# Kernel tuning notes

Measured on AMD Instinct MI355X. Metric: run time of the kernel, lower is better.

Reference implementation:

```python
import jax, jax.numpy as jnp
import numpy as np

HEADS = 16

def setup_inputs() -> dict:
    key = jax.random.key(0)
    ks = jax.random.split(key, 12)
    S, E = 2048, 1024
    x = jax.random.normal(ks[0], (S, E), dtype=jnp.float32)
    seg = jnp.sort(jax.random.randint(ks[1], (S,), 0, 32)).astype(jnp.int32)
    sc = 1.0 / np.sqrt(E)
    Wq = jax.random.normal(ks[2], (E, E), dtype=jnp.float32) * sc
    bq = jax.random.normal(ks[3], (E,), dtype=jnp.float32) * 0.01
    Wk = jax.random.normal(ks[4], (E, E), dtype=jnp.float32) * sc
    bk = jax.random.normal(ks[5], (E,), dtype=jnp.float32) * 0.01
    Wv = jax.random.normal(ks[6], (E, E), dtype=jnp.float32) * sc
    bv = jax.random.normal(ks[7], (E,), dtype=jnp.float32) * 0.01
    Wo = jax.random.normal(ks[8], (E, E), dtype=jnp.float32) * sc
    bo = jax.random.normal(ks[9], (E,), dtype=jnp.float32) * 0.01
    return {"x": x, "seg": seg, "pos": 1000,
            "Wq": Wq, "bq": bq, "Wk": Wk, "bk": bk,
            "Wv": Wv, "bv": bv, "Wo": Wo, "bo": bo}

def reference(x, seg, pos, Wq, bq, Wk, bk, Wv, bv, Wo, bo):
    S, E = x.shape
    H = HEADS
    d = E // H
    # projections: [S,E] -> [H,S,d]
    q = (x @ Wq + bq).reshape(S, H, d).transpose(1, 0, 2)
    k = (x @ Wk + bk).reshape(S, H, d).transpose(1, 0, 2)
    v = (x @ Wv + bv).reshape(S, H, d).transpose(1, 0, 2)
    # raw scores (note: original code applies NO 1/sqrt(d) scaling)
    scores = jnp.einsum('hid,hjd->hij', q, k)  # [H,S,S]
    same_seg = seg[:, None] == seg[None, :]    # [S,S]
    # faithful to original: out-of-segment entries stay ZERO (not -inf)
    scores = jnp.where(same_seg[None, :, :], scores, 0.0)
    weights = jax.nn.softmax(scores, axis=-1)
    out = jnp.einsum('hij,hjd->hid', weights, v)          # [H,S,d]
    out = out.transpose(1, 0, 2).reshape(S, E)            # [S,E]
    result = out @ Wo + bo                                # [S,E]
    # mean over the segment containing `pos`
    m = (seg == seg[pos]).astype(result.dtype)            # [S]
    return (result * m[:, None]).sum(axis=0) / m.sum()
```

## Files before the change

### kernel.cpp

```cpp
#include <hip/hip_runtime.h>

#define SS 2048
#define EE 1024
#define NH 16
#define DH 64
#define NR 128


__device__ __forceinline__ void fma4v(float4& a, const float4 xv,
                                      const float4 w0, const float4 w1,
                                      const float4 w2, const float4 w3) {
    a.x += xv.x * w0.x + xv.y * w1.x + xv.z * w2.x + xv.w * w3.x;
    a.y += xv.x * w0.y + xv.y * w1.y + xv.z * w2.y + xv.w * w3.y;
    a.z += xv.x * w0.z + xv.y * w1.z + xv.z * w2.z + xv.w * w3.z;
    a.w += xv.x * w0.w + xv.y * w1.w + xv.z * w2.w + xv.w * w3.w;
}

__device__ __forceinline__ void lgkm_wait() {
    asm volatile("s_waitcnt lgkmcnt(0)" ::: "memory");
}

__device__ __forceinline__ int2 seg_bounds(const int* __restrict__ seg,
                                           const int* __restrict__ pos) {
    __shared__ int sb[8];
    int t = threadIdx.x;
    int g = seg[pos[0]];
    int lomin = SS, himax = 0;
    const int4* s4 = (const int4*)seg;
#pragma unroll
    for (int i = t; i < SS / 4; i += 256) {
        int4 v = s4[i];
        int b = i * 4;
        if (v.x == g) { lomin = min(lomin, b);     himax = max(himax, b + 1); }
        if (v.y == g) { lomin = min(lomin, b + 1); himax = max(himax, b + 2); }
        if (v.z == g) { lomin = min(lomin, b + 2); himax = max(himax, b + 3); }
        if (v.w == g) { lomin = min(lomin, b + 3); himax = max(himax, b + 4); }
    }
    for (int o = 32; o; o >>= 1) {
        lomin = min(lomin, __shfl_xor(lomin, o, 64));
        himax = max(himax, __shfl_xor(himax, o, 64));
    }
    if ((t & 63) == 0) { sb[t >> 6] = lomin; sb[4 + (t >> 6)] = himax; }
    __syncthreads();
    return make_int2(min(min(sb[0], sb[1]), min(sb[2], sb[3])),
                     max(max(sb[4], sb[5]), max(sb[6], sb[7])));
}

__global__ void __launch_bounds__(256, 4) k_d1(
    const float* __restrict__ x, const int* __restrict__ seg,
    const int* __restrict__ pos,
    const float* __restrict__ Wq, const float* __restrict__ bq,
    const float* __restrict__ Wk, const float* __restrict__ bk,
    const float* __restrict__ Wv, const float* __restrict__ bv,
    float* __restrict__ xpart,
    float* __restrict__ Q, float* __restrict__ K, float* __restrict__ V,
    int nmax) {
    __shared__ float lds[4096];
    const int t = threadIdx.x, wv = t >> 6, lane = t & 63;

    if (blockIdx.z == 0) {
        int xb = blockIdx.y * 16 + blockIdx.x;
        if (xb >= 64) return;
        const float4* x4 = (const float4*)x + (size_t)(xb * 32) * 256 + t;
        float4 a = make_float4(0.f, 0.f, 0.f, 0.f);
#pragma unroll 8
        for (int r = 0; r < 32; ++r) {
            float4 v = x4[(size_t)r * 256];
            a.x += v.x; a.y += v.y; a.z += v.z; a.w += v.w;
        }
        ((float4*)(xpart + (size_t)xb * EE))[t] = a;
        return;
    }

    int2 bnd = seg_bounds(seg, pos);
    int lo = bnd.x;
    int nc = bnd.y - lo; if (nc > nmax) nc = nmax; if (nc < 1) nc = 1;
    int r0 = blockIdx.y * 4;
    if (r0 >= nc) return;
    int mat = blockIdx.z - 1;
    const float* W  = mat == 0 ? Wq : mat == 1 ? Wk : Wv;
    const float* bb = mat == 0 ? bq : mat == 1 ? bk : bv;
    float* dst      = mat == 0 ? Q  : mat == 1 ? K  : V;
    int e = blockIdx.x * 64 + lane;

    float (*xs)[1024] = (float(*)[1024])lds;
    int rw = r0 + wv; if (rw >= nc) rw = nc - 1;
    {
        const float4* src = (const float4*)(x + (size_t)(lo + rw) * EE);
        float4* dl = (float4*)&xs[wv][0];
#pragma unroll
        for (int i = 0; i < 4; ++i)
            dl[i * 64 + lane] = src[i * 64 + lane];
    }
    __syncthreads();

    const float* Wp = W + (size_t)(wv * 256) * EE + e;
    const float* x0 = &xs[0][wv * 256];
    const float* x1 = &xs[1][wv * 256];
    const float* x2 = &xs[2][wv * 256];
    const float* x3 = &xs[3][wv * 256];
    float a0 = 0.f, a1 = 0.f, a2 = 0.f, a3 = 0.f;
#pragma unroll 8
    for (int c = 0; c < 256; ++c) {
        float wj = Wp[(size_t)c * EE];
        a0 += x0[c] * wj;
        a1 += x1[c] * wj;
        a2 += x2[c] * wj;
        a3 += x3[c] * wj;
    }
    __syncthreads();

    float* red = lds;
    red[(wv * 4 + 0) * 64 + lane] = a0;
    red[(wv * 4 + 1) * 64 + lane] = a1;
    red[(wv * 4 + 2) * 64 + lane] = a2;
    red[(wv * 4 + 3) * 64 + lane] = a3;
    __syncthreads();
    float s = red[(0 * 4 + wv) * 64 + lane] + red[(1 * 4 + wv) * 64 + lane]
            + red[(2 * 4 + wv) * 64 + lane] + red[(3 * 4 + wv) * 64 + lane]
            + bb[e];
    int gr = r0 + wv;
    if (gr < nc)
        dst[(size_t)gr * EE + e] = s;
}

__global__ void __launch_bounds__(256, 4) k_d2(
    const int* __restrict__ seg, const int* __restrict__ pos,
    const float* __restrict__ Wv, const float* __restrict__ bv,
    const float* __restrict__ xpart,
    const float* __restrict__ Q, const float* __restrict__ K,
    const float* __restrict__ V,
    float* __restrict__ vtot, float* __restrict__ A, float* __restrict__ Bh,
    int nmax) {
    __shared__ float lds[2048];
    const int t = threadIdx.x, wv = t >> 6, lane = t & 63;
    const int bid = blockIdx.x, gb = gridDim.x;

    if (bid < 4) {
        float4 a = make_float4(0.f, 0.f, 0.f, 0.f);
        const float4* xp4 = (const float4*)xpart + t;
#pragma unroll 8
        for (int b = 0; b < 64; ++b) {
            float4 v = xp4[(size_t)b * 256];
            a.x += v.x; a.y += v.y; a.z += v.z; a.w += v.w;
        }
        ((float4*)lds)[t] = a;
        __syncthreads();
        int ct = bid;
        int e0 = ct * 256 + lane * 4;
        const float* Wp = Wv + (size_t)(wv * 256) * EE + e0;
        const float* xs = lds + wv * 256;
        float4 acc = make_float4(0.f, 0.f, 0.f, 0.f);
#pragma unroll 2
        for (int c = 0; c < 256; c += 4) {
            float4 w0 = *(const float4*)(Wp + (size_t)(c + 0) * EE);
            float4 w1 = *(const float4*)(Wp + (size_t)(c + 1) * EE);
            float4 w2 = *(const float4*)(Wp + (size_t)(c + 2) * EE);
            float4 w3 = *(const float4*)(Wp + (size_t)(c + 3) * EE);
            float4 xv = *(const float4*)(xs + c);
            fma4v(acc, xv, w0, w1, w2, w3);
        }
        *(float4*)(lds + 1024 + wv * 256 + lane * 4) = acc;
        __syncthreads();
        if (t < 64) {
            int oc = t * 4;
            float4 s0 = *(float4*)(lds + 1024 + 0 * 256 + oc);
            float4 s1 = *(float4*)(lds + 1024 + 1 * 256 + oc);
            float4 s2 = *(float4*)(lds + 1024 + 2 * 256 + oc);
            float4 s3 = *(float4*)(lds + 1024 + 3 * 256 + oc);
            float4 bvv = *(const float4*)(bv + ct * 256 + oc);
            float4 s;
            s.x = s0.x + s1.x + s2.x + s3.x + bvv.x * (float)SS;
            s.y = s0.y + s1.y + s2.y + s3.y + bvv.y * (float)SS;
            s.z = s0.z + s1.z + s2.z + s3.z + bvv.z * (float)SS;
            s.w = s0.w + s1.w + s2.w + s3.w + bvv.w * (float)SS;
            *(float4*)(vtot + ct * 256 + oc) = s;
        }
        return;
    }

    int2 bnd = seg_bounds(seg, pos);
    int nc = bnd.y - bnd.x; if (nc > nmax) nc = nmax; if (nc < 1) nc = 1;
    int nit = nc * NH;
    float* ql = lds + wv * 512;
    float* sb = ql + 64;
    for (int it = (bid - 4) * 4 + wv; it < nit; it += (gb - 4) * 4) {
        int r = it >> 4, h = it & 15;
        ql[lane] = Q[(size_t)r * EE + h * DH + lane];
        lgkm_wait();
        const float4* q4 = (const float4*)ql;
        float m = 0.f;
        for (int j = lane; j < nc; j += 64) {
            const float4* kr = (const float4*)(K + (size_t)j * EE + h * DH);
            float s = 0.f;
#pragma unroll 4
            for (int d = 0; d < DH / 4; ++d) {
                float4 kv = kr[d];
                float4 qv = q4[d];
                s += qv.x * kv.x + qv.y * kv.y + qv.z * kv.z + qv.w * kv.w;
            }
            sb[j] = s;
            m = fmaxf(m, s);
        }
        for (int o = 32; o; o >>= 1) m = fmaxf(m, __shfl_xor(m, o, 64));
        float dl = 0.f;
        for (int j = lane; j < nc; j += 64) {
            float wgt = __expf(sb[j] - m);
            sb[j] = wgt;
            dl += wgt;
        }
        for (int o = 32; o; o >>= 1) dl += __shfl_xor(dl, o, 64);
        float em = __expf(-m);
        float denom = dl + (float)(SS - nc) * em;
        lgkm_wait();
        float acc = 0.f, vs = 0.f;
        const float* Vp = V + h * DH + lane;
        int j = 0;
        for (; j + 4 <= nc; j += 4) {
            float4 wq = *(const float4*)(sb + j);
            float v0 = Vp[(size_t)(j + 0) * EE];
            float v1 = Vp[(size_t)(j + 1) * EE];
            float v2 = Vp[(size_t)(j + 2) * EE];
            float v3 = Vp[(size_t)(j + 3) * EE];
            acc += wq.x * v0 + wq.y * v1 + wq.z * v2 + wq.w * v3;
            vs  += v0 + v1 + v2 + v3;
        }
        for (; j < nc; ++j) {
            float v0 = Vp[(size_t)j * EE];
            acc += sb[j] * v0;
            vs  += v0;
        }
        atomicAdd(&A[h * DH + lane], (acc - vs * em) / denom);
        if (lane == 0) atomicAdd(&Bh[h], em / denom);
    }
}

__global__ void __launch_bounds__(256, 2) k_d3(
    const int* __restrict__ seg, const int* __restrict__ pos,
    const float* __restrict__ Wo, const float* __restrict__ bo,
    const float* __restrict__ vtot, const float* __restrict__ A,
    const float* __restrict__ Bh, int nmax, float* __restrict__ out) {
    __shared__ float lds[2048];
    const int t = threadIdx.x, wv = t >> 6, lane = t & 63;
    int2 bnd = seg_bounds(seg, pos);
    int nc = bnd.y - bnd.x; if (nc > nmax) nc = nmax; if (nc < 1) nc = 1;
    {
        float4 av = ((const float4*)A)[t];
        float4 vv = ((const float4*)vtot)[t];
        float bh = Bh[t >> 4];
        float4 o4;
        o4.x = av.x + vv.x * bh;
        o4.y = av.y + vv.y * bh;
        o4.z = av.z + vv.z * bh;
        o4.w = av.w + vv.w * bh;
        ((float4*)lds)[t] = o4;
    }
    __syncthreads();
    int ct = blockIdx.x;
    int e0 = ct * 256 + lane * 4;
    const float* Wp = Wo + (size_t)(wv * 256) * EE + e0;
    const float* osp = lds + wv * 256;
    float4 a = make_float4(0.f, 0.f, 0.f, 0.f);
#pragma unroll 2
    for (int c = 0; c < 256; c += 4) {
        float4 w0 = *(const float4*)(Wp + (size_t)(c + 0) * EE);
        float4 w1 = *(const float4*)(Wp + (size_t)(c + 1) * EE);
        float4 w2 = *(const float4*)(Wp + (size_t)(c + 2) * EE);
        float4 w3 = *(const float4*)(Wp + (size_t)(c + 3) * EE);
        float4 ov = *(const float4*)(osp + c);
        fma4v(a, ov, w0, w1, w2, w3);
    }
    *(float4*)(lds + 1024 + wv * 256 + lane * 4) = a;
    __syncthreads();
    if (t < 64) {
        int oc = t * 4;
        float4 s0 = *(float4*)(lds + 1024 + 0 * 256 + oc);
        float4 s1 = *(float4*)(lds + 1024 + 1 * 256 + oc);
        float4 s2 = *(float4*)(lds + 1024 + 2 * 256 + oc);
        float4 s3 = *(float4*)(lds + 1024 + 3 * 256 + oc);
        float inv = 1.f / (float)nc;
        float4 bov = *(const float4*)(bo + ct * 256 + oc);
        float4 o;
        o.x = bov.x + (s0.x + s1.x + s2.x + s3.x) * inv;
        o.y = bov.y + (s0.y + s1.y + s2.y + s3.y) * inv;
        o.z = bov.z + (s0.z + s1.z + s2.z + s3.z) * inv;
        o.w = bov.w + (s0.w + s1.w + s2.w + s3.w) * inv;
        *(float4*)(out + ct * 256 + oc) = o;
    }
}

extern "C" void kernel_launch(void* const* d_in, const int* in_sizes, int n_in,
                              void* d_out, int out_size, void* d_ws, size_t ws_size,
                              hipStream_t stream) {
    const float* x  = (const float*)d_in[0];
    const int* seg  = (const int*)d_in[1];
    const int* pos  = (const int*)d_in[2];
    const float* Wq = (const float*)d_in[3];
    const float* bq = (const float*)d_in[4];
    const float* Wk = (const float*)d_in[5];
    const float* bk = (const float*)d_in[6];
    const float* Wv = (const float*)d_in[7];
    const float* bv = (const float*)d_in[8];
    const float* Wo = (const float*)d_in[9];
    const float* bo = (const float*)d_in[10];
    float* out = (float*)d_out;

    char* w = (char*)d_ws;
    float* vtot  = (float*)(w + 0);
    float* A     = (float*)(w + 4096);
    float* Bh    = (float*)(w + 8192);
    float* xpart = (float*)(w + 16384);

    size_t base = 16384 + 64 * EE * sizeof(float);
    size_t avail = (ws_size > base) ? ws_size - base : 0;
    int nmax = (int)(avail / (3ull * EE * sizeof(float)));
    if (nmax > NR) nmax = NR;
    if (nmax < 1) nmax = 1;
    float* Q = (float*)(w + base);
    float* K = Q + (size_t)nmax * EE;
    float* V = K + (size_t)nmax * EE;

    int RT = (nmax + 3) / 4;
    int RY = RT > 4 ? RT : 4;

    hipMemsetAsync(w + 4096, 0, 8192, stream);
    k_d1<<<dim3(16, RY, 4), 256, 0, stream>>>(
        x, seg, pos, Wq, bq, Wk, bk, Wv, bv, xpart, Q, K, V, nmax);
    k_d2<<<260, 256, 0, stream>>>(
        seg, pos, Wv, bv, xpart, Q, K, V, vtot, A, Bh, nmax);
    k_d3<<<4, 256, 0, stream>>>(seg, pos, Wo, bo, vtot, A, Bh, nmax, out);
}
```

Measured before the change: 157.3 us.

## Replace x partial-sum buffer with atomics, precompute segment bounds, widen d2/d3 grids

The column sum of x is now accumulated with global atomics into one vector instead of 64 partial rows that k_d2 had to reduce. A dedicated block in k_d1 computes the segment bounds once and stores them in workspace, so k_d2 and k_d3 no longer rescan seg. The QKV projection reads x rows straight from global memory with wave-uniform addresses rather than staging them in LDS, and it loops over row tiles on a fixed 16-row-tile grid. The Wv and Wo matvecs are split over 16 blocks of 64 columns each, up from 4 blocks, to spread the weight streaming across more CUs. This adds atomic contention and makes the floating-point summation order nondeterministic.

Result: no change. 157.6 us (+0.2%).

```diff
diff --git a/kernel.cpp b/kernel.cpp
--- a/kernel.cpp
+++ b/kernel.cpp
@@ -7,17 +7,8 @@
 #define NR 128
 
 
-__device__ __forceinline__ void fma4v(float4& a, const float4 xv,
-                                      const float4 w0, const float4 w1,
-                                      const float4 w2, const float4 w3) {
-    a.x += xv.x * w0.x + xv.y * w1.x + xv.z * w2.x + xv.w * w3.x;
-    a.y += xv.x * w0.y + xv.y * w1.y + xv.z * w2.y + xv.w * w3.y;
-    a.z += xv.x * w0.z + xv.y * w1.z + xv.z * w2.z + xv.w * w3.z;
-    a.w += xv.x * w0.w + xv.y * w1.w + xv.z * w2.w + xv.w * w3.w;
-}
-
-__device__ __forceinline__ void lgkm_wait() {
-    asm volatile("s_waitcnt lgkmcnt(0)" ::: "memory");
+__device__ __forceinline__ int rfl(int v) {
+    return __builtin_amdgcn_readfirstlane(v);
 }
 
 __device__ __forceinline__ int2 seg_bounds(const int* __restrict__ seg,
@@ -52,82 +43,82 @@
     const float* __restrict__ Wq, const float* __restrict__ bq,
     const float* __restrict__ Wk, const float* __restrict__ bk,
     const float* __restrict__ Wv, const float* __restrict__ bv,
-    float* __restrict__ xpart,
+    float* __restrict__ xsum, int* __restrict__ meta,
     float* __restrict__ Q, float* __restrict__ K, float* __restrict__ V,
     int nmax) {
-    __shared__ float lds[4096];
+    __shared__ float red[1024];
     const int t = threadIdx.x, wv = t >> 6, lane = t & 63;
 
     if (blockIdx.z == 0) {
         int xb = blockIdx.y * 16 + blockIdx.x;
-        if (xb >= 64) return;
-        const float4* x4 = (const float4*)x + (size_t)(xb * 32) * 256 + t;
-        float4 a = make_float4(0.f, 0.f, 0.f, 0.f);
+        if (xb < 64) {
+            const float4* x4 = (const float4*)x + (size_t)(xb * 32) * 256 + t;
+            float4 a = make_float4(0.f, 0.f, 0.f, 0.f);
 #pragma unroll 8
-        for (int r = 0; r < 32; ++r) {
-            float4 v = x4[(size_t)r * 256];
-            a.x += v.x; a.y += v.y; a.z += v.z; a.w += v.w;
-        }
-        ((float4*)(xpart + (size_t)xb * EE))[t] = a;
+            for (int r = 0; r < 32; ++r) {
+                float4 v = x4[(size_t)r * 256];
+                a.x += v.x; a.y += v.y; a.z += v.z; a.w += v.w;
+            }
+            int e0 = 4 * t;
+            atomicAdd(&xsum[e0 + 0], a.x);
+            atomicAdd(&xsum[e0 + 1], a.y);
+            atomicAdd(&xsum[e0 + 2], a.z);
+            atomicAdd(&xsum[e0 + 3], a.w);
+        } else if (xb == 64) {
+            int2 bnd = seg_bounds(seg, pos);
+            if (t == 0) { meta[0] = bnd.x; meta[1] = bnd.y; }
+        }
         return;
     }
 
     int2 bnd = seg_bounds(seg, pos);
     int lo = bnd.x;
     int nc = bnd.y - lo; if (nc > nmax) nc = nmax; if (nc < 1) nc = 1;
-    int r0 = blockIdx.y * 4;
-    if (r0 >= nc) return;
     int mat = blockIdx.z - 1;
     const float* W  = mat == 0 ? Wq : mat == 1 ? Wk : Wv;
     const float* bb = mat == 0 ? bq : mat == 1 ? bk : bv;
     float* dst      = mat == 0 ? Q  : mat == 1 ? K  : V;
     int e = blockIdx.x * 64 + lane;
-
-    float (*xs)[1024] = (float(*)[1024])lds;
-    int rw = r0 + wv; if (rw >= nc) rw = nc - 1;
-    {
-        const float4* src = (const float4*)(x + (size_t)(lo + rw) * EE);
-        float4* dl = (float4*)&xs[wv][0];
-#pragma unroll
-        for (int i = 0; i < 4; ++i)
-            dl[i * 64 + lane] = src[i * 64 + lane];
-    }
-    __syncthreads();
-
-    const float* Wp = W + (size_t)(wv * 256) * EE + e;
-    const float* x0 = &xs[0][wv * 256];
-    const float* x1 = &xs[1][wv * 256];
-    const float* x2 = &xs[2][wv * 256];
-    const float* x3 = &xs[3][wv * 256];
-    float a0 = 0.f, a1 = 0.f, a2 = 0.f, a3 = 0.f;
+    int kbu = rfl(wv) * 256;
+    const float* Wp = W + (size_t)kbu * EE + e;
+    float bias = bb[e];
+
+    for (int rt = blockIdx.y; rt * 4 < nc; rt += 16) {
+        int r0 = rt * 4;
+        int rB = min(r0 + 1, nc - 1);
+        int rC = min(r0 + 2, nc - 1);
+        int rD = min(r0 + 3, nc - 1);
+        const float* xA = x + (size_t)rfl(lo + r0) * EE + kbu;
+        const float* xB = x + (size_t)rfl(lo + rB) * EE + kbu;
+        const float* xC = x + (size_t)rfl(lo + rC) * EE + kbu;
+        const float* xD = x + (size_t)rfl(lo + rD) * EE + kbu;
+        float a0 = 0.f, a1 = 0.f, a2 = 0.f, a3 = 0.f;
 #pragma unroll 8
-    for (int c = 0; c < 256; ++c) {
-        float wj = Wp[(size_t)c * EE];
-        a0 += x0[c] * wj;
-        a1 += x1[c] * wj;
-        a2 += x2[c] * wj;
-        a3 += x3[c] * wj;
-    }
-    __syncthreads();
-
-    float* red = lds;
-    red[(wv * 4 + 0) * 64 + lane] = a0;
-    red[(wv * 4 + 1) * 64 + lane] = a1;
-    red[(wv * 4 + 2) * 64 + lane] = a2;
-    red[(wv * 4 + 3) * 64 + lane] = a3;
-    __syncthreads();
-    float s = red[(0 * 4 + wv) * 64 + lane] + red[(1 * 4 + wv) * 64 + lane]
-            + red[(2 * 4 + wv) * 64 + lane] + red[(3 * 4 + wv) * 64 + lane]
-            + bb[e];
-    int gr = r0 + wv;
-    if (gr < nc)
-        dst[(size_t)gr * EE + e] = s;
+        for (int c = 0; c < 256; ++c) {
+            float wj = Wp[(size_t)c * EE];
+            a0 += xA[c] * wj;
+            a1 += xB[c] * wj;
+            a2 += xC[c] * wj;
+            a3 += xD[c] * wj;
+        }
+        __syncthreads();
+        red[(wv * 4 + 0) * 64 + lane] = a0;
+        red[(wv * 4 + 1) * 64 + lane] = a1;
+        red[(wv * 4 + 2) * 64 + lane] = a2;
+        red[(wv * 4 + 3) * 64 + lane] = a3;
+        __syncthreads();
+        float s = red[(0 * 4 + wv) * 64 + lane] + red[(1 * 4 + wv) * 64 + lane]
+                + red[(2 * 4 + wv) * 64 + lane] + red[(3 * 4 + wv) * 64 + lane]
+                + bias;
+        int gr = r0 + wv;
+        if (gr < nc)
+            dst[(size_t)gr * EE + e] = s;
+    }
 }
 
 __global__ void __launch_bounds__(256, 4) k_d2(
-    const int* __restrict__ seg, const int* __restrict__ pos,
     const float* __restrict__ Wv, const float* __restrict__ bv,
-    const float* __restrict__ xpart,
+    const float* __restrict__ xsum, const int* __restrict__ meta,
     const float* __restrict__ Q, const float* __restrict__ K,
     const float* __restrict__ V,
     float* __restrict__ vtot, float* __restrict__ A, float* __restrict__ Bh,
@@ -136,58 +127,42 @@
     const int t = threadIdx.x, wv = t >> 6, lane = t & 63;
     const int bid = blockIdx.x, gb = gridDim.x;
 
-    if (bid < 4) {
-        float4 a = make_float4(0.f, 0.f, 0.f, 0.f);
-        const float4* xp4 = (const float4*)xpart + t;
-#pragma unroll 8
-        for (int b = 0; b < 64; ++b) {
-            float4 v = xp4[(size_t)b * 256];
-            a.x += v.x; a.y += v.y; a.z += v.z; a.w += v.w;
-        }
-        ((float4*)lds)[t] = a;
-        __syncthreads();
-        int ct = bid;
-        int e0 = ct * 256 + lane * 4;
-        const float* Wp = Wv + (size_t)(wv * 256) * EE + e0;
-        const float* xs = lds + wv * 256;
-        float4 acc = make_float4(0.f, 0.f, 0.f, 0.f);
-#pragma unroll 2
+    if (bid < 16) {
+        ((float4*)lds)[t] = ((const float4*)xsum)[t];
+        __syncthreads();
+        int e = bid * 64 + lane;
+        int kbu = rfl(wv) * 256;
+        const float* Wp = Wv + (size_t)kbu * EE + e;
+        const float4* xs4 = (const float4*)(lds + kbu);
+        float a = 0.f;
+#pragma unroll 4
         for (int c = 0; c < 256; c += 4) {
-            float4 w0 = *(const float4*)(Wp + (size_t)(c + 0) * EE);
-            float4 w1 = *(const float4*)(Wp + (size_t)(c + 1) * EE);
-            float4 w2 = *(const float4*)(Wp + (size_t)(c + 2) * EE);
-            float4 w3 = *(const float4*)(Wp + (size_t)(c + 3) * EE);
-            float4 xv = *(const float4*)(xs + c);
-            fma4v(acc, xv, w0, w1, w2, w3);
-        }
-        *(float4*)(lds + 1024 + wv * 256 + lane * 4) = acc;
-        __syncthreads();
-        if (t < 64) {
-            int oc = t * 4;
-            float4 s0 = *(float4*)(lds + 1024 + 0 * 256 + oc);
-            float4 s1 = *(float4*)(lds + 1024 + 1 * 256 + oc);
-            float4 s2 = *(float4*)(lds + 1024 + 2 * 256 + oc);
-            float4 s3 = *(float4*)(lds + 1024 + 3 * 256 + oc);
-            float4 bvv = *(const float4*)(bv + ct * 256 + oc);
-            float4 s;
-            s.x = s0.x + s1.x + s2.x + s3.x + bvv.x * (float)SS;
-            s.y = s0.y + s1.y + s2.y + s3.y + bvv.y * (float)SS;
-            s.z = s0.z + s1.z + s2.z + s3.z + bvv.z * (float)SS;
-            s.w = s0.w + s1.w + s2.w + s3.w + bvv.w * (float)SS;
-            *(float4*)(vtot + ct * 256 + oc) = s;
+            float4 xv = xs4[c >> 2];
+            a += xv.x * Wp[(size_t)(c + 0) * EE]
+               + xv.y * Wp[(size_t)(c + 1) * EE]
+               + xv.z * Wp[(size_t)(c + 2) * EE]
+               + xv.w * Wp[(size_t)(c + 3) * EE];
+        }
+        __syncthreads();
+        lds[1024 + wv * 64 + lane] = a;
+        __syncthreads();
+        if (wv == 0) {
+            float s = lds[1024 + lane] + lds[1088 + lane]
+                    + lds[1152 + lane] + lds[1216 + lane];
+            vtot[e] = s + bv[e] * (float)SS;
         }
         return;
     }
 
-    int2 bnd = seg_bounds(seg, pos);
-    int nc = bnd.y - bnd.x; if (nc > nmax) nc = nmax; if (nc < 1) nc = 1;
+    int lo = meta[0];
+    int nc = meta[1] - lo; if (nc > nmax) nc = nmax; if (nc < 1) nc = 1;
     int nit = nc * NH;
     float* ql = lds + wv * 512;
     float* sb = ql + 64;
-    for (int it = (bid - 4) * 4 + wv; it < nit; it += (gb - 4) * 4) {
+    for (int it = (bid - 16) * 4 + wv; it < nit; it += (gb - 16) * 4) {
         int r = it >> 4, h = it & 15;
         ql[lane] = Q[(size_t)r * EE + h * DH + lane];
-        lgkm_wait();
+        asm volatile("s_waitcnt lgkmcnt(0)" ::: "memory");
         const float4* q4 = (const float4*)ql;
         float m = 0.f;
         for (int j = lane; j < nc; j += 64) {
@@ -212,7 +187,7 @@
         for (int o = 32; o; o >>= 1) dl += __shfl_xor(dl, o, 64);
         float em = __expf(-m);
         float denom = dl + (float)(SS - nc) * em;
-        lgkm_wait();
+        asm volatile("s_waitcnt lgkmcnt(0)" ::: "memory");
         float acc = 0.f, vs = 0.f;
         const float* Vp = V + h * DH + lane;
         int j = 0;
@@ -235,15 +210,14 @@
     }
 }
 
-__global__ void __launch_bounds__(256, 2) k_d3(
-    const int* __restrict__ seg, const int* __restrict__ pos,
+__global__ void __launch_bounds__(256, 4) k_d3(
+    const int* __restrict__ meta,
     const float* __restrict__ Wo, const float* __restrict__ bo,
     const float* __restrict__ vtot, const float* __restrict__ A,
     const float* __restrict__ Bh, int nmax, float* __restrict__ out) {
-    __shared__ float lds[2048];
+    __shared__ float lds[1344];
     const int t = threadIdx.x, wv = t >> 6, lane = t & 63;
-    int2 bnd = seg_bounds(seg, pos);
-    int nc = bnd.y - bnd.x; if (nc > nmax) nc = nmax; if (nc < 1) nc = 1;
+    int nc = meta[1] - meta[0]; if (nc > nmax) nc = nmax; if (nc < 1) nc = 1;
     {
         float4 av = ((const float4*)A)[t];
         float4 vv = ((const float4*)vtot)[t];
@@ -256,36 +230,26 @@
         ((float4*)lds)[t] = o4;
     }
     __syncthreads();
-    int ct = blockIdx.x;
-    int e0 = ct * 256 + lane * 4;
-    const float* Wp = Wo + (size_t)(wv * 256) * EE + e0;
-    const float* osp = lds + wv * 256;
-    float4 a = make_float4(0.f, 0.f, 0.f, 0.f);
-#pragma unroll 2
+    int e = blockIdx.x * 64 + lane;
+    int kbu = rfl(wv) * 256;
+    const float* Wp = Wo + (size_t)kbu * EE + e;
+    const float4* os4 = (const float4*)(lds + kbu);
+    float a = 0.f;
+#pragma unroll 4
     for (int c = 0; c < 256; c += 4) {
-        float4 w0 = *(const float4*)(Wp + (size_t)(c + 0) * EE);
-        float4 w1 = *(const float4*)(Wp + (size_t)(c + 1) * EE);
-        float4 w2 = *(const float4*)(Wp + (size_t)(c + 2) * EE);
-        float4 w3 = *(const float4*)(Wp + (size_t)(c + 3) * EE);
-        float4 ov = *(const float4*)(osp + c);
-        fma4v(a, ov, w0, w1, w2, w3);
-    }
-    *(float4*)(lds + 1024 + wv * 256 + lane * 4) = a;
-    __syncthreads();
-    if (t < 64) {
-        int oc = t * 4;
-        float4 s0 = *(float4*)(lds + 1024 + 0 * 256 + oc);
-        float4 s1 = *(float4*)(lds + 1024 + 1 * 256 + oc);
-        float4 s2 = *(float4*)(lds + 1024 + 2 * 256 + oc);
-        float4 s3 = *(float4*)(lds + 1024 + 3 * 256 + oc);
-        float inv = 1.f / (float)nc;
-        float4 bov = *(const float4*)(bo + ct * 256 + oc);
-        float4 o;
-        o.x = bov.x + (s0.x + s1.x + s2.x + s3.x) * inv;
-        o.y = bov.y + (s0.y + s1.y + s2.y + s3.y) * inv;
-        o.z = bov.z + (s0.z + s1.z + s2.z + s3.z) * inv;
-        o.w = bov.w + (s0.w + s1.w + s2.w + s3.w) * inv;
-        *(float4*)(out + ct * 256 + oc) = o;
+        float4 ov = os4[c >> 2];
+        a += ov.x * Wp[(size_t)(c + 0) * EE]
+           + ov.y * Wp[(size_t)(c + 1) * EE]
+           + ov.z * Wp[(size_t)(c + 2) * EE]
+           + ov.w * Wp[(size_t)(c + 3) * EE];
+    }
+    __syncthreads();
+    lds[1024 + wv * 64 + lane] = a;
+    __syncthreads();
+    if (wv == 0) {
+        float s = lds[1024 + lane] + lds[1088 + lane]
+                + lds[1152 + lane] + lds[1216 + lane];
+        out[e] = bo[e] + s / (float)nc;
     }
 }
 
@@ -306,12 +270,13 @@
     float* out = (float*)d_out;
 
     char* w = (char*)d_ws;
-    float* vtot  = (float*)(w + 0);
-    float* A     = (float*)(w + 4096);
-    float* Bh    = (float*)(w + 8192);
-    float* xpart = (float*)(w + 16384);
-
-    size_t base = 16384 + 64 * EE * sizeof(float);
+    float* xsum = (float*)(w + 0);
+    float* A    = (float*)(w + 4096);
+    float* Bh   = (float*)(w + 8192);
+    int*   meta = (int*)(w + 8256);
+    float* vtot = (float*)(w + 12288);
+
+    size_t base = 16384;
     size_t avail = (ws_size > base) ? ws_size - base : 0;
     int nmax = (int)(avail / (3ull * EE * sizeof(float)));
     if (nmax > NR) nmax = NR;
@@ -320,13 +285,10 @@
     float* K = Q + (size_t)nmax * EE;
     float* V = K + (size_t)nmax * EE;
 
-    int RT = (nmax + 3) / 4;
-    int RY = RT > 4 ? RT : 4;
-
-    hipMemsetAsync(w + 4096, 0, 8192, stream);
-    k_d1<<<dim3(16, RY, 4), 256, 0, stream>>>(
-        x, seg, pos, Wq, bq, Wk, bk, Wv, bv, xpart, Q, K, V, nmax);
-    k_d2<<<260, 256, 0, stream>>>(
-        seg, pos, Wv, bv, xpart, Q, K, V, vtot, A, Bh, nmax);
-    k_d3<<<4, 256, 0, stream>>>(seg, pos, Wo, bo, vtot, A, Bh, nmax, out);
-}
+    hipMemsetAsync(w, 0, 8264, stream);
+    k_d1<<<dim3(16, 16, 4), 256, 0, stream>>>(
+        x, seg, pos, Wq, bq, Wk, bk, Wv, bv, xsum, meta, Q, K, V, nmax);
+    k_d2<<<272, 256, 0, stream>>>(
+        Wv, bv, xsum, meta, Q, K, V, vtot, A, Bh, nmax);
+    k_d3<<<16, 256, 0, stream>>>(meta, Wo, bo, vtot, A, Bh, nmax, out);
+}
```
